# Performance work log

Hardware: AMD Instinct MI355X
Metric: run time of the kernel (lower is better)

## Reference

```python
import jax, jax.numpy as jnp
import numpy as np

B, S, H = 8, 4096, 512

def setup_inputs() -> dict:
    key = jax.random.key(0)
    k1, k2 = jax.random.split(key)
    lstm_out = jax.random.normal(k1, (B, S, H), dtype=jnp.float32)
    W = jax.random.normal(k2, (2 * H, H), dtype=jnp.float32) * (1.0 / np.sqrt(H))
    b = jnp.zeros((2 * H,), dtype=jnp.float32)
    return {"lstm_out": lstm_out, "W": W, "b": b}

def reference(lstm_out, W, b):
    # noise_net: Linear(H, 2H) + Softplus
    noise = jax.nn.softplus(jnp.einsum('bsh,oh->bso', lstm_out, W) + b)  # [B,S,2H]
    Q = noise[:, :, :H]   # process noise
    R = noise[:, :, H:]   # observation noise

    def step(carry, inp):
        state, P = carry
        z, q, r = inp                      # each [B,H]
        P_pred = P + q
        K = P_pred / (P_pred + r + 1e-6)
        state = state + K * (z - state)
        P = (1.0 - K) * P_pred
        return (state, P), state

    state0 = lstm_out[:, 0, :]
    P0 = jnp.full_like(state0, 0.1)
    # time-major for scan: [S,B,H]
    xs = (jnp.swapaxes(lstm_out, 0, 1),
          jnp.swapaxes(Q, 0, 1),
          jnp.swapaxes(R, 0, 1))
    _, states = jax.lax.scan(step, (state0, P0), xs)  # [S,B,H]
    return jnp.swapaxes(states, 0, 1)  # [B,S,H]
```

## Files before the change

### kernel.cpp

```cpp
#include <hip/hip_runtime.h>
#include <hip/hip_bf16.h>

#define B_ 8
#define S_ 4096
#define H_ 512

using short8 = __attribute__((ext_vector_type(8))) short;
using f32x4  = __attribute__((ext_vector_type(4))) float;

__device__ __forceinline__ float bf2f(unsigned u16) {
    return __uint_as_float(u16 << 16);
}
__device__ __forceinline__ unsigned pk2bf(float x, float y) {
    __hip_bfloat162 h = __float22bfloat162_rn(make_float2(x, y));
    return *reinterpret_cast<unsigned*>(&h);
}
__device__ __forceinline__ float softplus_f(float x) {
    float sp = __logf(1.0f + __expf(x));
    return x > 15.0f ? x : sp;
}

typedef __attribute__((address_space(1))) void* gbl_ptr_t;
typedef __attribute__((address_space(3))) void* lds_ptr_t;
__device__ __forceinline__ void gload_lds16(const void* g, void* l) {
    __builtin_amdgcn_global_load_lds((gbl_ptr_t)g, (lds_ptr_t)l, 16, 0, 0);
}

#define BAR() do { asm volatile("" ::: "memory"); \
                   __builtin_amdgcn_s_barrier(); \
                   asm volatile("" ::: "memory"); } while (0)

#define ASZ4 4194304u
#define TOT4 4325376u

__global__ __launch_bounds__(256)
void convert_bf16(const float* __restrict__ A, const float* __restrict__ Wm,
                  uint2* __restrict__ dst) {
    for (unsigned i = blockIdx.x * 256u + threadIdx.x; i < TOT4; i += 2048u * 256u) {
        const float4* p = (i < ASZ4) ? ((const float4*)A) + i
                                     : ((const float4*)Wm) + (i - ASZ4);
        const float4 v = *p;
        uint2 o;
        o.x = pk2bf(v.x, v.y);
        o.y = pk2bf(v.z, v.w);
        dst[i] = o;
    }
}

#define TM 128
#define TN 128
#define BK 32

__global__ __launch_bounds__(256, 4)
void gemm_softplus(const unsigned short* __restrict__ Ab,
                   const unsigned short* __restrict__ Wb,
                   const float* __restrict__ bias,
                   unsigned* __restrict__ QR) {
    __shared__ unsigned short As[2][4096];
    __shared__ unsigned short Bs[2][4096];

    const int bid     = blockIdx.x;
    const int logical = (bid & 7) * 256 + (bid >> 3);
    const int bm = logical >> 3;
    const int bn = logical & 7;

    const int t    = threadIdx.x;
    const int wave = t >> 6;
    const int lane = t & 63;
    const int wm  = (wave >> 1) * 64;
    const int wn  = (wave & 1) * 64;
    const int l15 = lane & 15;
    const int l4  = lane >> 4;

    const int m0 = bm * TM;

    const int lr2  = lane >> 2;
    const int s_st = (lr2 + (lane >> 4)) & 3;
    const int sg   = ((lane & 3) ^ s_st) * 8;
    const int row0 = wave * 16 + lr2;
    const int nr0 = bn * 64 + (row0 & 31) + ((row0 & 64) >> 1) + ((row0 & 32) << 4);
    const unsigned short* ag0 = Ab + (size_t)(m0 + row0) * 512 + sg;
    const unsigned short* bg0 = Wb + (size_t)nr0 * 512 + sg;
    const unsigned short* ag1 = ag0 + (size_t)64 * 512;
    const unsigned short* bg1 = bg0 + (size_t)32 * 512;
    const int sd0 = wave * 512;
    const int sd1 = sd0 + 2048;

    const int s_rd = (l15 + (l15 >> 2)) & 3;
    const int gsw  = (l4 ^ s_rd) * 8;
    const int aoff = (wm + l15) * 32 + gsw;
    const int boff = (wn + l15) * 32 + gsw;

    f32x4 acc[4][4] = {};

#define STAGE(s) do { \
    const int _sl = (s) & 1; const int _kc = (s) * BK; \
    gload_lds16(ag0 + _kc, &As[_sl][sd0]); \
    gload_lds16(ag1 + _kc, &As[_sl][sd1]); \
    gload_lds16(bg0 + _kc, &Bs[_sl][sd0]); \
    gload_lds16(bg1 + _kc, &Bs[_sl][sd1]); \
} while (0)

#define SLICE(g, VMN, DOSTG) do { \
    const unsigned short* _a = &As[(g) & 1][0]; \
    const unsigned short* _b = &Bs[(g) & 1][0]; \
    if (DOSTG) STAGE((g) + 1); \
    asm volatile("s_waitcnt vmcnt(" #VMN ")" ::: "memory"); \
    BAR(); \
    short8 af[4], bf[4]; \
    _Pragma("unroll") for (int i = 0; i < 4; ++i) { \
        af[i] = *(const short8*)(_a + aoff + i * 512); \
        bf[i] = *(const short8*)(_b + boff + i * 512); \
    } \
    __builtin_amdgcn_s_setprio(1); \
    _Pragma("unroll") for (int i = 0; i < 4; ++i) \
    _Pragma("unroll") for (int j = 0; j < 4; ++j) \
        acc[i][j] = __builtin_amdgcn_mfma_f32_16x16x32_bf16(af[i], bf[j], acc[i][j], 0, 0, 0); \
    __builtin_amdgcn_s_setprio(0); \
    BAR(); \
} while (0)

    STAGE(0);
    for (int g = 0; g < 15; ++g) {
        SLICE(g, 4, 1);
    }
    SLICE(15, 0, 0);

#undef SLICE
#undef STAGE

#pragma unroll
    for (int j = 0; j < 2; ++j) {
        const int h  = bn * 64 + (wn >> 1) + j * 16 + l15;
        const float bq = bias[h];
        const float br = bias[h + 512];
#pragma unroll
        for (int i = 0; i < 4; ++i) {
            const int mb = m0 + wm + i * 16 + l4 * 4;
#pragma unroll
            for (int r = 0; r < 4; ++r) {
                const float qv = softplus_f(acc[i][j][r] + bq);
                const float rv = softplus_f(acc[i][j + 2][r] + br);
                QR[(size_t)(mb + r) * 512 + h] = pk2bf(qv, rv);
            }
        }
    }
}

#define CHUNK 128
#define WARM 64

__global__ __launch_bounds__(256, 2)
void kalman_scan(const float* __restrict__ z,
                 const unsigned* __restrict__ QR,
                 float* __restrict__ out) {
    const int t     = threadIdx.x;
    const int hb    = blockIdx.x & 1;
    const int b     = (blockIdx.x >> 1) & 7;
    const int chunk = blockIdx.x >> 4;
    const int h     = hb * 256 + t;
    const int s0    = chunk << 7;
    const int sw    = (chunk == 0) ? 0 : (s0 - WARM);
    const size_t base = ((size_t)(b * S_ + sw)) * 512 + h;

    const float*    zp  = z + base;
    const unsigned* qrp = (const unsigned*)QR + base;
    float*          op  = out + base;

    const int ng    = ((s0 + CHUNK) - sw) >> 3;
    const int skipg = (s0 - sw) >> 3;

    float    Z0[8], Z1[8], Z2[8], Z3[8], Z4[8], Z5[8], Z6[8], Z7[8];
    unsigned Q0[8], Q1[8], Q2[8], Q3[8], Q4[8], Q5[8], Q6[8], Q7[8];

#define LOADG(g, Zb, Qb) { const int _o = (g) * 8;                          \
    _Pragma("unroll") for (int u = 0; u < 8; ++u) {                         \
        Zb[u] = zp[(size_t)(_o + u) * 512]; Qb[u] = qrp[(size_t)(_o + u) * 512]; } }

#define COMP(g, Zb, Qb) { const int _o = (g) * 8; const bool _st = (g) >= skipg; \
    _Pragma("unroll") for (int u = 0; u < 8; ++u) {                         \
        const float q  = bf2f(Qb[u] & 0xffffu);                             \
        const float r  = bf2f(Qb[u] >> 16);                                 \
        const float Pp = P + q, rr = r + 1e-6f;                             \
        const float K  = Pp * __builtin_amdgcn_rcpf(Pp + rr);               \
        state = fmaf(K, Zb[u] - state, state); P = rr * K;                  \
        if (_st) op[(size_t)(_o + u) * 512] = state; } }

    LOADG(0, Z0, Q0); LOADG(1, Z1, Q1); LOADG(2, Z2, Q2); LOADG(3, Z3, Q3);

    float state = Z0[0];
    float P = 0.1f;

    for (int g = 0; g < ng; g += 8) {
        if (g + 4  < ng) LOADG(g + 4,  Z4, Q4); COMP(g,     Z0, Q0);
        if (g + 5  < ng) LOADG(g + 5,  Z5, Q5); COMP(g + 1, Z1, Q1);
        if (g + 6  < ng) LOADG(g + 6,  Z6, Q6); COMP(g + 2, Z2, Q2);
        if (g + 7  < ng) LOADG(g + 7,  Z7, Q7); COMP(g + 3, Z3, Q3);
        if (g + 8  < ng) LOADG(g + 8,  Z0, Q0); COMP(g + 4, Z4, Q4);
        if (g + 9  < ng) LOADG(g + 9,  Z1, Q1); COMP(g + 5, Z5, Q5);
        if (g + 10 < ng) LOADG(g + 10, Z2, Q2); COMP(g + 6, Z6, Q6);
        if (g + 11 < ng) LOADG(g + 11, Z3, Q3); COMP(g + 7, Z7, Q7);
    }
#undef LOADG
#undef COMP
}

extern "C" void kernel_launch(void* const* d_in, const int* in_sizes, int n_in,
                              void* d_out, int out_size, void* d_ws, size_t ws_size,
                              hipStream_t stream) {
    const float* lstm = (const float*)d_in[0];
    const float* Wm   = (const float*)d_in[1];
    const float* bias = (const float*)d_in[2];

    unsigned* QRw = (unsigned*)d_ws;

    unsigned short* Abf = (unsigned short*)d_out;
    unsigned short* Wbf = (unsigned short*)((char*)d_out + (32u << 20));

    hipLaunchKernelGGL(convert_bf16, dim3(2048), dim3(256), 0, stream,
                       lstm, Wm, (uint2*)Abf);

    hipLaunchKernelGGL(gemm_softplus, dim3(2048), dim3(256), 0, stream,
                       Abf, Wbf, bias, QRw);

    hipLaunchKernelGGL(kalman_scan, dim3(512), dim3(256), 0, stream,
                       lstm, QRw, (float*)d_out);
}
```

Measured before the change: 201.6 us.

## Enlarge GEMM tiles to 256x256 with 512-thread blocks and 8x4 wave tiles

The bf16 GEMM tile grows from 128x128 to 256x256, with 8 waves per block. Each wave now computes a 128x64 sub-tile (8x4 MFMA accumulators), and the grid shrinks from 2048 to 512 blocks. The aim is higher arithmetic intensity per LDS load and less global/L2 traffic per output element. In exchange it doubles accumulator registers and LDS per block, which may cut occupancy, and 512 blocks give fewer waves of work across the CUs.

```diff
diff --git a/kernel.cpp b/kernel.cpp
--- a/kernel.cpp
+++ b/kernel.cpp
@@ -47,28 +47,30 @@
     }
 }
 
-#define TM 128
-#define TN 128
+#define TM 256
+#define TN 256
 #define BK 32
 
-__global__ __launch_bounds__(256, 4)
+__global__ __launch_bounds__(512, 2)
 void gemm_softplus(const unsigned short* __restrict__ Ab,
                    const unsigned short* __restrict__ Wb,
                    const float* __restrict__ bias,
                    unsigned* __restrict__ QR) {
-    __shared__ unsigned short As[2][4096];
-    __shared__ unsigned short Bs[2][4096];
+    __shared__ unsigned short As[2][8192];
+    __shared__ unsigned short Bs[2][8192];
 
     const int bid     = blockIdx.x;
-    const int logical = (bid & 7) * 256 + (bid >> 3);
-    const int bm = logical >> 3;
-    const int bn = logical & 7;
-
-    const int t    = threadIdx.x;
-    const int wave = t >> 6;
-    const int lane = t & 63;
-    const int wm  = (wave >> 1) * 64;
-    const int wn  = (wave & 1) * 64;
+    const int logical = (bid & 7) * 64 + (bid >> 3);
+    const int bm = logical >> 2;
+    const int bn = logical & 3;
+
+    const int t      = threadIdx.x;
+    const int wave   = t >> 6;
+    const int lane   = t & 63;
+    const int wave_m = wave >> 2;
+    const int wave_n = wave & 3;
+    const int wm  = wave_m * 128;
+    const int wn  = wave_n * 64;
     const int l15 = lane & 15;
     const int l4  = lane >> 4;
 
@@ -78,27 +80,26 @@
     const int s_st = (lr2 + (lane >> 4)) & 3;
     const int sg   = ((lane & 3) ^ s_st) * 8;
     const int row0 = wave * 16 + lr2;
-    const int nr0 = bn * 64 + (row0 & 31) + ((row0 & 64) >> 1) + ((row0 & 32) << 4);
-    const unsigned short* ag0 = Ab + (size_t)(m0 + row0) * 512 + sg;
-    const unsigned short* bg0 = Wb + (size_t)nr0 * 512 + sg;
-    const unsigned short* ag1 = ag0 + (size_t)64 * 512;
-    const unsigned short* bg1 = bg0 + (size_t)32 * 512;
-    const int sd0 = wave * 512;
-    const int sd1 = sd0 + 2048;
+    const int nr0 = bn * 128 + ((row0 >> 6) << 5) + (row0 & 31) + (((row0 >> 5) & 1) << 9);
+    const unsigned short* agA0 = Ab + (size_t)(m0 + row0) * 512 + sg;
+    const unsigned short* agA1 = agA0 + (size_t)128 * 512;
+    const unsigned short* bgB0 = Wb + (size_t)nr0 * 512 + sg;
+    const unsigned short* bgB1 = bgB0 + (size_t)64 * 512;
+    const int sd = wave * 512;
 
     const int s_rd = (l15 + (l15 >> 2)) & 3;
     const int gsw  = (l4 ^ s_rd) * 8;
     const int aoff = (wm + l15) * 32 + gsw;
     const int boff = (wn + l15) * 32 + gsw;
 
-    f32x4 acc[4][4] = {};
+    f32x4 acc[8][4] = {};
 
 #define STAGE(s) do { \
     const int _sl = (s) & 1; const int _kc = (s) * BK; \
-    gload_lds16(ag0 + _kc, &As[_sl][sd0]); \
-    gload_lds16(ag1 + _kc, &As[_sl][sd1]); \
-    gload_lds16(bg0 + _kc, &Bs[_sl][sd0]); \
-    gload_lds16(bg1 + _kc, &Bs[_sl][sd1]); \
+    gload_lds16(agA0 + _kc, &As[_sl][sd]); \
+    gload_lds16(agA1 + _kc, &As[_sl][sd + 4096]); \
+    gload_lds16(bgB0 + _kc, &Bs[_sl][sd]); \
+    gload_lds16(bgB1 + _kc, &Bs[_sl][sd + 4096]); \
 } while (0)
 
 #define SLICE(g, VMN, DOSTG) do { \
@@ -107,13 +108,13 @@
     if (DOSTG) STAGE((g) + 1); \
     asm volatile("s_waitcnt vmcnt(" #VMN ")" ::: "memory"); \
     BAR(); \
-    short8 af[4], bf[4]; \
-    _Pragma("unroll") for (int i = 0; i < 4; ++i) { \
+    short8 af[8], bf[4]; \
+    _Pragma("unroll") for (int j = 0; j < 4; ++j) \
+        bf[j] = *(const short8*)(_b + boff + j * 512); \
+    _Pragma("unroll") for (int i = 0; i < 8; ++i) \
         af[i] = *(const short8*)(_a + aoff + i * 512); \
-        bf[i] = *(const short8*)(_b + boff + i * 512); \
-    } \
     __builtin_amdgcn_s_setprio(1); \
-    _Pragma("unroll") for (int i = 0; i < 4; ++i) \
+    _Pragma("unroll") for (int i = 0; i < 8; ++i) \
     _Pragma("unroll") for (int j = 0; j < 4; ++j) \
         acc[i][j] = __builtin_amdgcn_mfma_f32_16x16x32_bf16(af[i], bf[j], acc[i][j], 0, 0, 0); \
     __builtin_amdgcn_s_setprio(0); \
@@ -131,11 +132,11 @@
 
 #pragma unroll
     for (int j = 0; j < 2; ++j) {
-        const int h  = bn * 64 + (wn >> 1) + j * 16 + l15;
+        const int h  = bn * 128 + (wn >> 1) + j * 16 + l15;
         const float bq = bias[h];
         const float br = bias[h + 512];
 #pragma unroll
-        for (int i = 0; i < 4; ++i) {
+        for (int i = 0; i < 8; ++i) {
             const int mb = m0 + wm + i * 16 + l4 * 4;
 #pragma unroll
             for (int r = 0; r < 4; ++r) {
@@ -220,7 +221,7 @@
     hipLaunchKernelGGL(convert_bf16, dim3(2048), dim3(256), 0, stream,
                        lstm, Wm, (uint2*)Abf);
 
-    hipLaunchKernelGGL(gemm_softplus, dim3(2048), dim3(256), 0, stream,
+    hipLaunchKernelGGL(gemm_softplus, dim3(512), dim3(512), 0, stream,
                        Abf, Wbf, bias, QRw);
 
     hipLaunchKernelGGL(kalman_scan, dim3(512), dim3(256), 0, stream,
```

After: 210.3 us. 1.04x slower.

## Fuse fp32-to-bf16 conversion into GEMM staging and enlarge Kalman scan chunks

Applied to the files above, without the earlier changes.

Removes the separate conversion kernel. The GEMM now loads fp32 A and W straight into registers, converts them to bf16 and writes them into padded LDS tiles, software-pipelined two stages ahead. This drops a full extra read/write pass over the 64MB input and one kernel launch, but GEMM global traffic doubles because it now reads fp32. The Kalman scan chunk also doubles to 256, halving the grid and reducing the redundant warm-up steps, at the cost of less parallelism.

```diff
diff --git a/kernel.cpp b/kernel.cpp
--- a/kernel.cpp
+++ b/kernel.cpp
@@ -20,44 +20,22 @@
     return x > 15.0f ? x : sp;
 }
 
-typedef __attribute__((address_space(1))) void* gbl_ptr_t;
-typedef __attribute__((address_space(3))) void* lds_ptr_t;
-__device__ __forceinline__ void gload_lds16(const void* g, void* l) {
-    __builtin_amdgcn_global_load_lds((gbl_ptr_t)g, (lds_ptr_t)l, 16, 0, 0);
-}
-
 #define BAR() do { asm volatile("" ::: "memory"); \
                    __builtin_amdgcn_s_barrier(); \
                    asm volatile("" ::: "memory"); } while (0)
 
-#define ASZ4 4194304u
-#define TOT4 4325376u
-
-__global__ __launch_bounds__(256)
-void convert_bf16(const float* __restrict__ A, const float* __restrict__ Wm,
-                  uint2* __restrict__ dst) {
-    for (unsigned i = blockIdx.x * 256u + threadIdx.x; i < TOT4; i += 2048u * 256u) {
-        const float4* p = (i < ASZ4) ? ((const float4*)A) + i
-                                     : ((const float4*)Wm) + (i - ASZ4);
-        const float4 v = *p;
-        uint2 o;
-        o.x = pk2bf(v.x, v.y);
-        o.y = pk2bf(v.z, v.w);
-        dst[i] = o;
-    }
-}
-
 #define TM 128
 #define TN 128
 #define BK 32
+#define LDT 40
 
 __global__ __launch_bounds__(256, 4)
-void gemm_softplus(const unsigned short* __restrict__ Ab,
-                   const unsigned short* __restrict__ Wb,
+void gemm_softplus(const float* __restrict__ Af,
+                   const float* __restrict__ Wf,
                    const float* __restrict__ bias,
                    unsigned* __restrict__ QR) {
-    __shared__ unsigned short As[2][4096];
-    __shared__ unsigned short Bs[2][4096];
+    __shared__ unsigned short As[2][TM * LDT];
+    __shared__ unsigned short Bs[2][TN * LDT];
 
     const int bid     = blockIdx.x;
     const int logical = (bid & 7) * 256 + (bid >> 3);
@@ -74,60 +52,79 @@
 
     const int m0 = bm * TM;
 
-    const int lr2  = lane >> 2;
-    const int s_st = (lr2 + (lane >> 4)) & 3;
-    const int sg   = ((lane & 3) ^ s_st) * 8;
-    const int row0 = wave * 16 + lr2;
-    const int nr0 = bn * 64 + (row0 & 31) + ((row0 & 64) >> 1) + ((row0 & 32) << 4);
-    const unsigned short* ag0 = Ab + (size_t)(m0 + row0) * 512 + sg;
-    const unsigned short* bg0 = Wb + (size_t)nr0 * 512 + sg;
-    const unsigned short* ag1 = ag0 + (size_t)64 * 512;
-    const unsigned short* bg1 = bg0 + (size_t)32 * 512;
-    const int sd0 = wave * 512;
-    const int sd1 = sd0 + 2048;
-
-    const int s_rd = (l15 + (l15 >> 2)) & 3;
-    const int gsw  = (l4 ^ s_rd) * 8;
-    const int aoff = (wm + l15) * 32 + gsw;
-    const int boff = (wn + l15) * 32 + gsw;
+    const int srow = t >> 1;
+    const int sh   = (t & 1) * 16;
+    const int nsr = bn * 64 + (srow & 31) + ((srow & 64) >> 1) + ((srow & 32) << 4);
+    const float* aS = Af + (size_t)(m0 + srow) * 512 + sh;
+    const float* bS = Wf + (size_t)nsr * 512 + sh;
+    unsigned short* aD0 = &As[0][srow * LDT + sh];
+    unsigned short* aD1 = &As[1][srow * LDT + sh];
+    unsigned short* bD0 = &Bs[0][srow * LDT + sh];
+    unsigned short* bD1 = &Bs[1][srow * LDT + sh];
+
+    const int aoff = (wm + l15) * LDT + l4 * 8;
+    const int boff = (wn + l15) * LDT + l4 * 8;
 
     f32x4 acc[4][4] = {};
-
-#define STAGE(s) do { \
-    const int _sl = (s) & 1; const int _kc = (s) * BK; \
-    gload_lds16(ag0 + _kc, &As[_sl][sd0]); \
-    gload_lds16(ag1 + _kc, &As[_sl][sd1]); \
-    gload_lds16(bg0 + _kc, &Bs[_sl][sd0]); \
-    gload_lds16(bg1 + _kc, &Bs[_sl][sd1]); \
+    float4 ra[4], rb[4];
+
+#define LOADREGS(s) do { \
+    const float4* _ap = (const float4*)(aS + (s) * BK); \
+    const float4* _bp = (const float4*)(bS + (s) * BK); \
+    _Pragma("unroll") for (int jj = 0; jj < 4; ++jj) { \
+        ra[jj] = _ap[jj]; rb[jj] = _bp[jj]; } \
 } while (0)
 
-#define SLICE(g, VMN, DOSTG) do { \
+#define CVTWRITE(s) do { \
+    unsigned short* _ad = ((s) & 1) ? aD1 : aD0; \
+    unsigned short* _bd = ((s) & 1) ? bD1 : bD0; \
+    uint4 w; \
+    w.x = pk2bf(ra[0].x, ra[0].y); w.y = pk2bf(ra[0].z, ra[0].w); \
+    w.z = pk2bf(ra[1].x, ra[1].y); w.w = pk2bf(ra[1].z, ra[1].w); \
+    *(uint4*)_ad = w; \
+    w.x = pk2bf(ra[2].x, ra[2].y); w.y = pk2bf(ra[2].z, ra[2].w); \
+    w.z = pk2bf(ra[3].x, ra[3].y); w.w = pk2bf(ra[3].z, ra[3].w); \
+    *(uint4*)(_ad + 8) = w; \
+    w.x = pk2bf(rb[0].x, rb[0].y); w.y = pk2bf(rb[0].z, rb[0].w); \
+    w.z = pk2bf(rb[1].x, rb[1].y); w.w = pk2bf(rb[1].z, rb[1].w); \
+    *(uint4*)_bd = w; \
+    w.x = pk2bf(rb[2].x, rb[2].y); w.y = pk2bf(rb[2].z, rb[2].w); \
+    w.z = pk2bf(rb[3].x, rb[3].y); w.w = pk2bf(rb[3].z, rb[3].w); \
+    *(uint4*)(_bd + 8) = w; \
+} while (0)
+
+#define PHASE(g, DW, DL) do { \
     const unsigned short* _a = &As[(g) & 1][0]; \
     const unsigned short* _b = &Bs[(g) & 1][0]; \
-    if (DOSTG) STAGE((g) + 1); \
-    asm volatile("s_waitcnt vmcnt(" #VMN ")" ::: "memory"); \
-    BAR(); \
     short8 af[4], bf[4]; \
-    _Pragma("unroll") for (int i = 0; i < 4; ++i) { \
-        af[i] = *(const short8*)(_a + aoff + i * 512); \
-        bf[i] = *(const short8*)(_b + boff + i * 512); \
+    _Pragma("unroll") for (int ii = 0; ii < 4; ++ii) { \
+        af[ii] = *(const short8*)(_a + aoff + ii * 16 * LDT); \
+        bf[ii] = *(const short8*)(_b + boff + ii * 16 * LDT); \
     } \
+    if (DW) CVTWRITE((g) + 1); \
+    if (DL) LOADREGS((g) + 2); \
     __builtin_amdgcn_s_setprio(1); \
-    _Pragma("unroll") for (int i = 0; i < 4; ++i) \
-    _Pragma("unroll") for (int j = 0; j < 4; ++j) \
-        acc[i][j] = __builtin_amdgcn_mfma_f32_16x16x32_bf16(af[i], bf[j], acc[i][j], 0, 0, 0); \
+    _Pragma("unroll") for (int ii = 0; ii < 4; ++ii) \
+    _Pragma("unroll") for (int jj = 0; jj < 4; ++jj) \
+        acc[ii][jj] = __builtin_amdgcn_mfma_f32_16x16x32_bf16(af[ii], bf[jj], acc[ii][jj], 0, 0, 0); \
     __builtin_amdgcn_s_setprio(0); \
+    asm volatile("s_waitcnt lgkmcnt(0)" ::: "memory"); \
     BAR(); \
 } while (0)
 
-    STAGE(0);
-    for (int g = 0; g < 15; ++g) {
-        SLICE(g, 4, 1);
-    }
-    SLICE(15, 0, 0);
-
-#undef SLICE
-#undef STAGE
+    LOADREGS(0);
+    CVTWRITE(0);
+    LOADREGS(1);
+    asm volatile("s_waitcnt lgkmcnt(0)" ::: "memory");
+    BAR();
+
+    for (int g = 0; g < 14; ++g) PHASE(g, 1, 1);
+    PHASE(14, 1, 0);
+    PHASE(15, 0, 0);
+
+#undef PHASE
+#undef CVTWRITE
+#undef LOADREGS
 
 #pragma unroll
     for (int j = 0; j < 2; ++j) {
@@ -147,7 +144,7 @@
     }
 }
 
-#define CHUNK 128
+#define CHUNK 256
 #define WARM 64
 
 __global__ __launch_bounds__(256, 2)
@@ -159,7 +156,7 @@
     const int b     = (blockIdx.x >> 1) & 7;
     const int chunk = blockIdx.x >> 4;
     const int h     = hb * 256 + t;
-    const int s0    = chunk << 7;
+    const int s0    = chunk << 8;
     const int sw    = (chunk == 0) ? 0 : (s0 - WARM);
     const size_t base = ((size_t)(b * S_ + sw)) * 512 + h;
 
@@ -214,15 +211,9 @@
 
     unsigned* QRw = (unsigned*)d_ws;
 
-    unsigned short* Abf = (unsigned short*)d_out;
-    unsigned short* Wbf = (unsigned short*)((char*)d_out + (32u << 20));
-
-    hipLaunchKernelGGL(convert_bf16, dim3(2048), dim3(256), 0, stream,
-                       lstm, Wm, (uint2*)Abf);
-
     hipLaunchKernelGGL(gemm_softplus, dim3(2048), dim3(256), 0, stream,
-                       Abf, Wbf, bias, QRw);
-
-    hipLaunchKernelGGL(kalman_scan, dim3(512), dim3(256), 0, stream,
+                       lstm, Wm, bias, QRw);
+
+    hipLaunchKernelGGL(kalman_scan, dim3(256), dim3(256), 0, stream,
                        lstm, QRw, (float*)d_out);
 }
```

Result: slower. 284.4 us (+41.1%).
